# Performance work log

Measured on AMD Instinct MI355X. Metric: run time of the kernel, lower is better.

The kernel has to match this reference:

```python
import jax, jax.numpy as jnp
import numpy as np

B, T, N, F_IN, F_OUT = 8, 64, 256, 128, 64
NEG_INF = -9e15


def setup_inputs() -> dict:
    key = jax.random.key(0)
    k_h, k_w, k_a, k_adj = jax.random.split(key, 4)
    h = jax.random.normal(k_h, (B, T, N, F_IN), dtype=jnp.float32)
    W = jax.random.normal(k_w, (F_IN, F_OUT), dtype=jnp.float32) * (1.414 / np.sqrt(F_IN))
    a = jax.random.normal(k_a, (2 * F_OUT, 1), dtype=jnp.float32) * 0.1
    # binary adjacency with guaranteed self-loops so every softmax row is valid
    adj = (jax.random.uniform(k_adj, (N, N)) > 0.5).astype(jnp.float32)
    adj = jnp.maximum(adj, jnp.eye(N, dtype=jnp.float32))
    return {"h": h, "W": W, "a": a, "adj": adj}


def reference(h, W, a, adj):
    # Wh: [B, T, N, F_OUT]
    Wh = jnp.einsum('btnf,fo->btno', h, W)
    a1 = a[:F_OUT, 0]   # [F_OUT]
    a2 = a[F_OUT:, 0]   # [F_OUT]
    Wh1 = jnp.einsum('btno,o->btn', Wh, a1)  # source scores
    Wh2 = jnp.einsum('btno,o->btn', Wh, a2)  # target scores
    # e: [B, T, N, N] = leakyrelu(Wh1_i + Wh2_j)
    e = jax.nn.leaky_relu(Wh1[..., :, None] + Wh2[..., None, :], negative_slope=0.01)
    attention = jnp.where(adj > 0, e, NEG_INF)
    alpha = jax.nn.softmax(attention, axis=-1)
    # dropout is identity at inference (training=False)
    h_prime = jnp.einsum('btnm,btmo->btno', alpha, Wh)
    return jax.nn.elu(h_prime)  # concat=True path
```

## Files before the change

### kernel.cpp

```cpp
#include <hip/hip_runtime.h>
#include <hip/hip_bf16.h>

#define NN 256
#define FI 128
#define FO 64
#define LOG2E 1.4426950408889634f

typedef short s16x8 __attribute__((ext_vector_type(8)));
typedef float f32x4 __attribute__((ext_vector_type(4)));

__device__ __forceinline__ unsigned f2bf1(float x) {
  union { float f; unsigned u; } v; v.f = x;
  unsigned r = v.u + 0x7FFFu + ((v.u >> 16) & 1u);
  return r >> 16;
}
__device__ __forceinline__ unsigned pack2(float a, float b) {
  return f2bf1(a) | (f2bf1(b) << 16);
}
__device__ __forceinline__ unsigned pktrunc(float lo, float hi) {
  union { float f; unsigned u; } a, b; a.f = hi; b.f = lo;
  return __builtin_amdgcn_perm(a.u, b.u, 0x07060302u);
}
__device__ __forceinline__ float fexp2(float x) {
#if __has_builtin(__builtin_amdgcn_exp2f)
  return __builtin_amdgcn_exp2f(x);
#else
  return exp2f(x);
#endif
}

__global__ __launch_bounds__(256) void gat_k0(const float* __restrict__ adj,
                                              unsigned* __restrict__ msk) {
  const int row = blockIdx.x;
  const int wv = threadIdx.x >> 6, lane = threadIdx.x & 63;
  float v = adj[row * NN + wv * 64 + lane];
  unsigned long long b = __ballot(v > 0.f);
  if (lane == 0) {
    msk[row * 8 + wv * 2]     = (unsigned)b;
    msk[row * 8 + wv * 2 + 1] = (unsigned)(b >> 32);
  }
}

__device__ __forceinline__ void phaseA_sub(
    const float4 (&x)[4][2], int w, int s, int m, int q,
    const unsigned short* sWT, const float* sA,
    unsigned short* sWhB, float* sWh1, float* sWh2)
{
  const int R = 32 * w + 16 * s;
  s16x8 af[4];
  #pragma unroll
  for (int kt = 0; kt < 4; ++kt) {
    union { unsigned u[4]; s16x8 v; } pk;
    pk.u[0] = pack2(x[kt][0].x, x[kt][0].y);
    pk.u[1] = pack2(x[kt][0].z, x[kt][0].w);
    pk.u[2] = pack2(x[kt][1].x, x[kt][1].y);
    pk.u[3] = pack2(x[kt][1].z, x[kt][1].w);
    af[kt] = pk.v;
  }
  f32x4 acc[4];
  #pragma unroll
  for (int nt = 0; nt < 4; ++nt) acc[nt] = (f32x4){0.f, 0.f, 0.f, 0.f};
  #pragma unroll
  for (int kt = 0; kt < 4; ++kt)
    #pragma unroll
    for (int nt = 0; nt < 4; ++nt) {
      s16x8 bf = *(const s16x8*)&sWT[(16 * nt + m) * 136 + kt * 32 + q * 8];
      acc[nt] = __builtin_amdgcn_mfma_f32_16x16x32_bf16(af[kt], bf, acc[nt], 0, 0, 0);
    }

  {
    float p1[4] = {0.f,0.f,0.f,0.f}, p2[4] = {0.f,0.f,0.f,0.f};
    #pragma unroll
    for (int nt = 0; nt < 4; ++nt) {
      float a1v = sA[16 * nt + m];
      float a2v = sA[FO + 16 * nt + m];
      #pragma unroll
      for (int r = 0; r < 4; ++r) { p1[r] += acc[nt][r] * a1v; p2[r] += acc[nt][r] * a2v; }
    }
    #pragma unroll
    for (int off = 1; off < 16; off <<= 1)
      #pragma unroll
      for (int r = 0; r < 4; ++r) {
        p1[r] += __shfl_xor(p1[r], off);
        p2[r] += __shfl_xor(p2[r], off);
      }
    if (m == 0) {
      *(float4*)&sWh1[R + 4 * q] =
          make_float4(p1[0]*LOG2E, p1[1]*LOG2E, p1[2]*LOG2E, p1[3]*LOG2E);
      *(float4*)&sWh2[R + 4 * q] =
          make_float4(p2[0]*LOG2E, p2[1]*LOG2E, p2[2]*LOG2E, p2[3]*LOG2E);
    }
  }
  {
    const int qB = (2 * s + (q >> 1)) & 3;
    #pragma unroll
    for (int nt = 0; nt < 4; ++nt) {
      int chunk = ((w * 4 + nt) * 16 + m) * 4 + (qB ^ (m & 3));
      uint2 wrv;
      wrv.x = pack2(acc[nt][0], acc[nt][1]);
      wrv.y = pack2(acc[nt][2], acc[nt][3]);
      *(uint2*)((char*)sWhB + chunk * 16 + (q & 1) * 8) = wrv;
    }
  }
}

__global__ __launch_bounds__(512)
__attribute__((amdgpu_waves_per_eu(3, 4)))
void gat_fused(
    const float* __restrict__ h, const float* __restrict__ W,
    const float* __restrict__ a, const unsigned* __restrict__ msk,
    float* __restrict__ out)
{
  const int bid  = blockIdx.x;
  const int bt   = bid >> 1;
  const int half = bid & 1;
  const int tid  = threadIdx.x;
  const int lane = tid & 63;
  const int w    = tid >> 6;
  const int m    = lane & 15;
  const int q    = lane >> 4;

  __shared__ __align__(16) unsigned short sWhB[64 * 256];
  __shared__ __align__(16) unsigned short sWT[64 * 136];
  __shared__ __align__(16) float sWh1[NN], sWh2[NN];
  __shared__ __align__(16) float sA[2 * FO];

  const float* __restrict__ hB = h + (size_t)bt * NN * FI;

  float4 x0[4][2];
  #pragma unroll
  for (int kt = 0; kt < 4; ++kt) {
    const float* p = hB + (size_t)(32 * w + m) * FI + kt * 32 + q * 8;
    x0[kt][0] = *(const float4*)p;
    x0[kt][1] = *(const float4*)(p + 4);
  }
  float4 x1[4][2];
  #pragma unroll
  for (int kt = 0; kt < 4; ++kt) {
    const float* p = hB + (size_t)(32 * w + 16 + m) * FI + kt * 32 + q * 8;
    x1[kt][0] = *(const float4*)p;
    x1[kt][1] = *(const float4*)(p + 4);
  }

  if (tid < 2 * FO) sA[tid] = a[tid];
  for (int idx = tid; idx < FI * FO; idx += 512) {
    int k = idx >> 6, o = idx & 63;
    sWT[o * 136 + k] = (unsigned short)f2bf1(W[idx]);
  }
  __syncthreads();

  phaseA_sub(x0, w, 0, m, q, sWT, sA, sWhB, sWh1, sWh2);
  phaseA_sub(x1, w, 1, m, q, sWT, sA, sWhB, sWh1, sWh2);
  __syncthreads();

  float* outB = out + (size_t)bt * NN * FO;
  {
    const int R2  = 128 * half + 16 * w;
    const int row = R2 + m;

    const uint4 mka = *(const uint4*)&msk[row * 8];
    const uint4 mkb = *(const uint4*)&msk[row * 8 + 4];
    const unsigned mkw[8] = {mka.x, mka.y, mka.z, mka.w, mkb.x, mkb.y, mkb.z, mkb.w};
    const float w1 = sWh1[row];

    s16x8 A[8];
    float sum = 0.f;
    #pragma unroll
    for (int kt = 0; kt < 8; ++kt) {
      int j0 = kt * 32 + q * 8;
      float4 w20 = *(const float4*)&sWh2[j0];
      float4 w21 = *(const float4*)&sWh2[j0 + 4];
      unsigned wq = mkw[kt] >> (q * 8);
      float p[8];
      const float w2e[8] = {w20.x, w20.y, w20.z, w20.w, w21.x, w21.y, w21.z, w21.w};
      #pragma unroll
      for (int e = 0; e < 8; ++e) {
        float l = w1 + w2e[e];
        l = fmaxf(l, 0.01f * l);
        union { float f; int i; } u_; u_.f = fexp2(l);
        u_.i &= ((int)(wq << (31 - e))) >> 31;
        p[e] = u_.f;
        sum += u_.f;
      }
      union { unsigned u[4]; s16x8 v; } pk;
      pk.u[0] = pktrunc(p[0], p[1]);
      pk.u[1] = pktrunc(p[2], p[3]);
      pk.u[2] = pktrunc(p[4], p[5]);
      pk.u[3] = pktrunc(p[6], p[7]);
      A[kt] = pk.v;
    }
    sum += __shfl_xor(sum, 16);
    sum += __shfl_xor(sum, 32);
    const float inv = __builtin_amdgcn_rcpf(sum);

    f32x4 acc[4];
    #pragma unroll
    for (int ot = 0; ot < 4; ++ot) acc[ot] = (f32x4){0.f, 0.f, 0.f, 0.f};
    #pragma unroll
    for (int kt = 0; kt < 8; ++kt) {
      #pragma unroll
      for (int ot = 0; ot < 4; ++ot) {
        int chunk = ((kt * 4 + ot) * 16 + m) * 4 + (q ^ (m & 3));
        s16x8 whf = *(const s16x8*)&sWhB[chunk * 8];
        acc[ot] = __builtin_amdgcn_mfma_f32_16x16x32_bf16(whf, A[kt], acc[ot], 0, 0, 0);
      }
    }

    #pragma unroll
    for (int ot = 0; ot < 4; ++ot) {
      float4 v4;
      float* vp = (float*)&v4;
      #pragma unroll
      for (int r = 0; r < 4; ++r) {
        float v = acc[ot][r] * inv;
        float ev = fexp2(v * LOG2E) - 1.f;
        vp[r] = v > 0.f ? v : ev;
      }
      *(float4*)&outB[row * FO + 16 * ot + 4 * q] = v4;
    }
  }
}

extern "C" void kernel_launch(void* const* d_in, const int* in_sizes, int n_in,
                              void* d_out, int out_size, void* d_ws, size_t ws_size,
                              hipStream_t stream) {
  const float* h   = (const float*)d_in[0];
  const float* W   = (const float*)d_in[1];
  const float* a   = (const float*)d_in[2];
  const float* adj = (const float*)d_in[3];
  float* out = (float*)d_out;

  unsigned* msk = (unsigned*)d_ws;

  gat_k0<<<dim3(256), dim3(256), 0, stream>>>(adj, msk);
  gat_fused<<<dim3(1024), dim3(512), 0, stream>>>(h, W, a, msk, out);
}
```

Before: 138.1 us.

## Split fused GAT kernel into projection and attention kernels via global workspace

Converts W to transposed bf16 once in the mask kernel instead of once per block. Splits the fused kernel into a projection kernel that writes bf16 Wh and the score vectors to global memory, and an attention kernel that reads them back. This removes the redundant per-block W conversion and the recomputation of Wh by both halves of each batch-time slice, and the smaller 256-thread blocks with no LDS should allow more blocks to run at once. The cost is a global round trip for Wh (about 8 MB each way), an extra launch, and attention-stage MFMA operands now loaded directly from global or cache instead of LDS.

```diff
diff --git a/kernel.cpp b/kernel.cpp
--- a/kernel.cpp
+++ b/kernel.cpp
@@ -30,23 +30,60 @@
 }
 
 __global__ __launch_bounds__(256) void gat_k0(const float* __restrict__ adj,
-                                              unsigned* __restrict__ msk) {
-  const int row = blockIdx.x;
-  const int wv = threadIdx.x >> 6, lane = threadIdx.x & 63;
-  float v = adj[row * NN + wv * 64 + lane];
-  unsigned long long b = __ballot(v > 0.f);
-  if (lane == 0) {
-    msk[row * 8 + wv * 2]     = (unsigned)b;
-    msk[row * 8 + wv * 2 + 1] = (unsigned)(b >> 32);
-  }
-}
-
-__device__ __forceinline__ void phaseA_sub(
-    const float4 (&x)[4][2], int w, int s, int m, int q,
-    const unsigned short* sWT, const float* sA,
-    unsigned short* sWhB, float* sWh1, float* sWh2)
+                                              const float* __restrict__ W,
+                                              unsigned* __restrict__ msk,
+                                              unsigned short* __restrict__ WTbf) {
+  const int b = blockIdx.x;
+  if (b < NN) {
+    const int row = b;
+    const int wv = threadIdx.x >> 6, lane = threadIdx.x & 63;
+    float v = adj[row * NN + wv * 64 + lane];
+    unsigned long long bb = __ballot(v > 0.f);
+    if (lane == 0) {
+      msk[row * 8 + wv * 2]     = (unsigned)bb;
+      msk[row * 8 + wv * 2 + 1] = (unsigned)(bb >> 32);
+    }
+  } else {
+    for (int idx = threadIdx.x; idx < FI * FO; idx += 256) {
+      int k = idx >> 6, o = idx & 63;
+      WTbf[o * FI + k] = (unsigned short)f2bf1(W[idx]);
+    }
+  }
+}
+
+__global__ __launch_bounds__(256, 4)
+void gat_wh(const float* __restrict__ h, const unsigned short* __restrict__ WTbf,
+            const float* __restrict__ a,
+            unsigned short* __restrict__ whG,
+            float* __restrict__ wh1G, float* __restrict__ wh2G)
 {
-  const int R = 32 * w + 16 * s;
+  const int bid  = blockIdx.x;
+  const int g    = bid >> 2;
+  const int qt   = bid & 3;
+  const int tid  = threadIdx.x;
+  const int lane = tid & 63;
+  const int w2   = tid >> 6;
+  const int m    = lane & 15;
+  const int q    = lane >> 4;
+  const int R    = 64 * qt + 16 * w2;
+
+  const float* __restrict__ hB = h + (size_t)g * NN * FI;
+
+  float4 x[4][2];
+  #pragma unroll
+  for (int kt = 0; kt < 4; ++kt) {
+    const float* p = hB + (size_t)(R + m) * FI + kt * 32 + q * 8;
+    x[kt][0] = *(const float4*)p;
+    x[kt][1] = *(const float4*)(p + 4);
+  }
+
+  float a1v[4], a2v[4];
+  #pragma unroll
+  for (int nt = 0; nt < 4; ++nt) {
+    a1v[nt] = a[16 * nt + m];
+    a2v[nt] = a[FO + 16 * nt + m];
+  }
+
   s16x8 af[4];
   #pragma unroll
   for (int kt = 0; kt < 4; ++kt) {
@@ -57,6 +94,7 @@
     pk.u[3] = pack2(x[kt][1].z, x[kt][1].w);
     af[kt] = pk.v;
   }
+
   f32x4 acc[4];
   #pragma unroll
   for (int nt = 0; nt < 4; ++nt) acc[nt] = (f32x4){0.f, 0.f, 0.f, 0.f};
@@ -64,7 +102,7 @@
   for (int kt = 0; kt < 4; ++kt)
     #pragma unroll
     for (int nt = 0; nt < 4; ++nt) {
-      s16x8 bf = *(const s16x8*)&sWT[(16 * nt + m) * 136 + kt * 32 + q * 8];
+      s16x8 bf = *(const s16x8*)&WTbf[(16 * nt + m) * FI + kt * 32 + q * 8];
       acc[nt] = __builtin_amdgcn_mfma_f32_16x16x32_bf16(af[kt], bf, acc[nt], 0, 0, 0);
     }
 
@@ -72,10 +110,8 @@
     float p1[4] = {0.f,0.f,0.f,0.f}, p2[4] = {0.f,0.f,0.f,0.f};
     #pragma unroll
     for (int nt = 0; nt < 4; ++nt) {
-      float a1v = sA[16 * nt + m];
-      float a2v = sA[FO + 16 * nt + m];
       #pragma unroll
-      for (int r = 0; r < 4; ++r) { p1[r] += acc[nt][r] * a1v; p2[r] += acc[nt][r] * a2v; }
+      for (int r = 0; r < 4; ++r) { p1[r] += acc[nt][r] * a1v[nt]; p2[r] += acc[nt][r] * a2v[nt]; }
     }
     #pragma unroll
     for (int off = 1; off < 16; off <<= 1)
@@ -85,139 +121,107 @@
         p2[r] += __shfl_xor(p2[r], off);
       }
     if (m == 0) {
-      *(float4*)&sWh1[R + 4 * q] =
+      *(float4*)&wh1G[g * NN + R + 4 * q] =
           make_float4(p1[0]*LOG2E, p1[1]*LOG2E, p1[2]*LOG2E, p1[3]*LOG2E);
-      *(float4*)&sWh2[R + 4 * q] =
+      *(float4*)&wh2G[g * NN + R + 4 * q] =
           make_float4(p2[0]*LOG2E, p2[1]*LOG2E, p2[2]*LOG2E, p2[3]*LOG2E);
     }
   }
+
   {
-    const int qB = (2 * s + (q >> 1)) & 3;
+    const int Wv = R >> 5;
+    const int S  = (R >> 4) & 1;
+    const int qB = (2 * S + (q >> 1)) & 3;
+    unsigned short* whP = whG + (size_t)g * (NN * FO);
     #pragma unroll
     for (int nt = 0; nt < 4; ++nt) {
-      int chunk = ((w * 4 + nt) * 16 + m) * 4 + (qB ^ (m & 3));
+      int chunk = ((Wv * 4 + nt) * 16 + m) * 4 + qB;
       uint2 wrv;
       wrv.x = pack2(acc[nt][0], acc[nt][1]);
       wrv.y = pack2(acc[nt][2], acc[nt][3]);
-      *(uint2*)((char*)sWhB + chunk * 16 + (q & 1) * 8) = wrv;
-    }
-  }
-}
-
-__global__ __launch_bounds__(512)
-__attribute__((amdgpu_waves_per_eu(3, 4)))
-void gat_fused(
-    const float* __restrict__ h, const float* __restrict__ W,
-    const float* __restrict__ a, const unsigned* __restrict__ msk,
-    float* __restrict__ out)
+      *(uint2*)((char*)whP + chunk * 16 + (q & 1) * 8) = wrv;
+    }
+  }
+}
+
+__global__ __launch_bounds__(256, 4)
+void gat_attn(const unsigned short* __restrict__ whG,
+              const float* __restrict__ wh1G, const float* __restrict__ wh2G,
+              const unsigned* __restrict__ msk, float* __restrict__ out)
 {
   const int bid  = blockIdx.x;
-  const int bt   = bid >> 1;
-  const int half = bid & 1;
+  const int g    = bid >> 2;
+  const int qt   = bid & 3;
   const int tid  = threadIdx.x;
   const int lane = tid & 63;
-  const int w    = tid >> 6;
+  const int w2   = tid >> 6;
   const int m    = lane & 15;
   const int q    = lane >> 4;
-
-  __shared__ __align__(16) unsigned short sWhB[64 * 256];
-  __shared__ __align__(16) unsigned short sWT[64 * 136];
-  __shared__ __align__(16) float sWh1[NN], sWh2[NN];
-  __shared__ __align__(16) float sA[2 * FO];
-
-  const float* __restrict__ hB = h + (size_t)bt * NN * FI;
-
-  float4 x0[4][2];
-  #pragma unroll
-  for (int kt = 0; kt < 4; ++kt) {
-    const float* p = hB + (size_t)(32 * w + m) * FI + kt * 32 + q * 8;
-    x0[kt][0] = *(const float4*)p;
-    x0[kt][1] = *(const float4*)(p + 4);
-  }
-  float4 x1[4][2];
-  #pragma unroll
-  for (int kt = 0; kt < 4; ++kt) {
-    const float* p = hB + (size_t)(32 * w + 16 + m) * FI + kt * 32 + q * 8;
-    x1[kt][0] = *(const float4*)p;
-    x1[kt][1] = *(const float4*)(p + 4);
-  }
-
-  if (tid < 2 * FO) sA[tid] = a[tid];
-  for (int idx = tid; idx < FI * FO; idx += 512) {
-    int k = idx >> 6, o = idx & 63;
-    sWT[o * 136 + k] = (unsigned short)f2bf1(W[idx]);
-  }
-  __syncthreads();
-
-  phaseA_sub(x0, w, 0, m, q, sWT, sA, sWhB, sWh1, sWh2);
-  phaseA_sub(x1, w, 1, m, q, sWT, sA, sWhB, sWh1, sWh2);
-  __syncthreads();
-
-  float* outB = out + (size_t)bt * NN * FO;
-  {
-    const int R2  = 128 * half + 16 * w;
-    const int row = R2 + m;
-
-    const uint4 mka = *(const uint4*)&msk[row * 8];
-    const uint4 mkb = *(const uint4*)&msk[row * 8 + 4];
-    const unsigned mkw[8] = {mka.x, mka.y, mka.z, mka.w, mkb.x, mkb.y, mkb.z, mkb.w};
-    const float w1 = sWh1[row];
-
-    s16x8 A[8];
-    float sum = 0.f;
-    #pragma unroll
-    for (int kt = 0; kt < 8; ++kt) {
-      int j0 = kt * 32 + q * 8;
-      float4 w20 = *(const float4*)&sWh2[j0];
-      float4 w21 = *(const float4*)&sWh2[j0 + 4];
-      unsigned wq = mkw[kt] >> (q * 8);
-      float p[8];
-      const float w2e[8] = {w20.x, w20.y, w20.z, w20.w, w21.x, w21.y, w21.z, w21.w};
-      #pragma unroll
-      for (int e = 0; e < 8; ++e) {
-        float l = w1 + w2e[e];
-        l = fmaxf(l, 0.01f * l);
-        union { float f; int i; } u_; u_.f = fexp2(l);
-        u_.i &= ((int)(wq << (31 - e))) >> 31;
-        p[e] = u_.f;
-        sum += u_.f;
-      }
-      union { unsigned u[4]; s16x8 v; } pk;
-      pk.u[0] = pktrunc(p[0], p[1]);
-      pk.u[1] = pktrunc(p[2], p[3]);
-      pk.u[2] = pktrunc(p[4], p[5]);
-      pk.u[3] = pktrunc(p[6], p[7]);
-      A[kt] = pk.v;
-    }
-    sum += __shfl_xor(sum, 16);
-    sum += __shfl_xor(sum, 32);
-    const float inv = __builtin_amdgcn_rcpf(sum);
-
-    f32x4 acc[4];
-    #pragma unroll
-    for (int ot = 0; ot < 4; ++ot) acc[ot] = (f32x4){0.f, 0.f, 0.f, 0.f};
-    #pragma unroll
-    for (int kt = 0; kt < 8; ++kt) {
-      #pragma unroll
-      for (int ot = 0; ot < 4; ++ot) {
-        int chunk = ((kt * 4 + ot) * 16 + m) * 4 + (q ^ (m & 3));
-        s16x8 whf = *(const s16x8*)&sWhB[chunk * 8];
-        acc[ot] = __builtin_amdgcn_mfma_f32_16x16x32_bf16(whf, A[kt], acc[ot], 0, 0, 0);
-      }
-    }
-
+  const int row  = 64 * qt + 16 * w2 + m;
+
+  const unsigned short* __restrict__ whP = whG + (size_t)g * (NN * FO);
+  const float* __restrict__ wh2B = wh2G + g * NN;
+
+  const uint4 mka = *(const uint4*)&msk[row * 8];
+  const uint4 mkb = *(const uint4*)&msk[row * 8 + 4];
+  const unsigned mkw[8] = {mka.x, mka.y, mka.z, mka.w, mkb.x, mkb.y, mkb.z, mkb.w};
+  const float w1 = wh1G[g * NN + row];
+
+  s16x8 A[8];
+  float sum = 0.f;
+  #pragma unroll
+  for (int kt = 0; kt < 8; ++kt) {
+    int j0 = kt * 32 + q * 8;
+    float4 w20 = *(const float4*)&wh2B[j0];
+    float4 w21 = *(const float4*)&wh2B[j0 + 4];
+    unsigned wq = mkw[kt] >> (q * 8);
+    float p[8];
+    const float w2e[8] = {w20.x, w20.y, w20.z, w20.w, w21.x, w21.y, w21.z, w21.w};
+    #pragma unroll
+    for (int e = 0; e < 8; ++e) {
+      float l = w1 + w2e[e];
+      l = fmaxf(l, 0.01f * l);
+      union { float f; int i; } u_; u_.f = fexp2(l);
+      u_.i &= ((int)(wq << (31 - e))) >> 31;
+      p[e] = u_.f;
+      sum += u_.f;
+    }
+    union { unsigned u[4]; s16x8 v; } pk;
+    pk.u[0] = pktrunc(p[0], p[1]);
+    pk.u[1] = pktrunc(p[2], p[3]);
+    pk.u[2] = pktrunc(p[4], p[5]);
+    pk.u[3] = pktrunc(p[6], p[7]);
+    A[kt] = pk.v;
+  }
+  sum += __shfl_xor(sum, 16);
+  sum += __shfl_xor(sum, 32);
+  const float inv = __builtin_amdgcn_rcpf(sum);
+
+  f32x4 acc[4];
+  #pragma unroll
+  for (int ot = 0; ot < 4; ++ot) acc[ot] = (f32x4){0.f, 0.f, 0.f, 0.f};
+  #pragma unroll
+  for (int kt = 0; kt < 8; ++kt) {
     #pragma unroll
     for (int ot = 0; ot < 4; ++ot) {
-      float4 v4;
-      float* vp = (float*)&v4;
-      #pragma unroll
-      for (int r = 0; r < 4; ++r) {
-        float v = acc[ot][r] * inv;
-        float ev = fexp2(v * LOG2E) - 1.f;
-        vp[r] = v > 0.f ? v : ev;
-      }
-      *(float4*)&outB[row * FO + 16 * ot + 4 * q] = v4;
-    }
+      int chunk = ((kt * 4 + ot) * 16 + m) * 4 + q;
+      s16x8 whf = *(const s16x8*)&whP[chunk * 8];
+      acc[ot] = __builtin_amdgcn_mfma_f32_16x16x32_bf16(whf, A[kt], acc[ot], 0, 0, 0);
+    }
+  }
+
+  float* outB = out + (size_t)g * NN * FO;
+  #pragma unroll
+  for (int ot = 0; ot < 4; ++ot) {
+    float4 v4;
+    float* vp = (float*)&v4;
+    #pragma unroll
+    for (int r = 0; r < 4; ++r) {
+      float v = acc[ot][r] * inv;
+      float ev = fexp2(v * LOG2E) - 1.f;
+      vp[r] = v > 0.f ? v : ev;
+    }
+    *(float4*)&outB[row * FO + 16 * ot + 4 * q] = v4;
   }
 }
 
@@ -230,8 +234,14 @@
   const float* adj = (const float*)d_in[3];
   float* out = (float*)d_out;
 
-  unsigned* msk = (unsigned*)d_ws;
-
-  gat_k0<<<dim3(256), dim3(256), 0, stream>>>(adj, msk);
-  gat_fused<<<dim3(1024), dim3(512), 0, stream>>>(h, W, a, msk, out);
-}
+  char* ws = (char*)d_ws;
+  unsigned*        msk  = (unsigned*)(ws);
+  unsigned short*  WTbf = (unsigned short*)(ws + 8192);
+  float*           wh1G = (float*)(ws + 8192 + 16384);
+  float*           wh2G = (float*)(ws + 8192 + 16384 + 524288);
+  unsigned short*  whG  = (unsigned short*)(ws + 8192 + 16384 + 2 * 524288);
+
+  gat_k0  <<<dim3(NN + 1), dim3(256), 0, stream>>>(adj, W, msk, WTbf);
+  gat_wh  <<<dim3(2048),   dim3(256), 0, stream>>>(h, WTbf, a, whG, wh1G, wh2G);
+  gat_attn<<<dim3(2048),   dim3(256), 0, stream>>>(whG, wh1G, wh2G, msk, out);
+}
```

Result: slower. 151.6 us (+9.8%).
